# Performance work log

Measured on AMD Instinct MI355X. Metric: run time of the kernel, lower is better.

The kernel has to match this reference:

```python
import jax, jax.numpy as jnp
import numpy as np

HEADS = 8
EPS = 1e-5


def setup_inputs() -> dict:
    key = jax.random.key(0)
    B, N, C = 32, 4096, 256
    headc = C // HEADS
    x = jax.random.normal(key, (B, N, C), dtype=jnp.float32)
    return {
        "x": x,
        "kln_weight": jnp.ones((HEADS, 1, headc), dtype=jnp.float32),
        "kln_bias": jnp.zeros((HEADS, 1, headc), dtype=jnp.float32),
        "vln_weight": jnp.ones((HEADS, 1, headc), dtype=jnp.float32),
        "vln_bias": jnp.zeros((HEADS, 1, headc), dtype=jnp.float32),
    }


def _ln(t, w, b, headc):
    # Faithful to the torch module: unbiased std (ddof=1), eps added to std (not var).
    m = jnp.mean(t, axis=-1, keepdims=True)
    d = t - m
    std = jnp.sqrt(jnp.sum(d * d, axis=-1, keepdims=True) / (headc - 1))
    return w * (d / (std + EPS)) + b


def reference(x, kln_weight, kln_bias, vln_weight, vln_bias):
    B, N, C = x.shape
    headc = C // HEADS
    # [B, H, N, D]
    qkv = x.reshape(B, N, HEADS, headc).transpose(0, 2, 1, 3)
    k = _ln(qkv, kln_weight, kln_bias, headc)
    v = _ln(qkv, vln_weight, vln_bias, headc)
    # k^T v : [B, H, D, D], scaled by 1/N
    kv = jnp.einsum("bhnd,bhne->bhde", k, v) / N
    # q (k^T v): [B, H, N, D]
    out = jnp.einsum("bhnd,bhde->bhne", qkv, kv)
    out = out.transpose(0, 2, 1, 3).reshape(B, N, C)
    return out + x
```

## Files before the change

### kernel.cpp

```cpp
#include <hip/hip_runtime.h>

#define H_ 8
#define D_ 32
#define B_ 32
#define N_ 4096
#define C_ 256
#define EPS_ 1e-5f

#define SLOT_ 1088

typedef __attribute__((ext_vector_type(8))) short bf16x8;
typedef __attribute__((ext_vector_type(4))) float f32x4;

__device__ __forceinline__ short f2bf(float f) {
    unsigned u = __builtin_bit_cast(unsigned, f);
    unsigned r = (u + 0x7FFFu + ((u >> 16) & 1u)) >> 16;
    return (short)r;
}
__device__ __forceinline__ float bf2f(short s) {
    return __builtin_bit_cast(float, ((unsigned)(unsigned short)s) << 16);
}

__device__ __forceinline__ int uidx(int r, int c) {
    return r * 40 + ((r >> 3) & 3) * 16 + c;
}

__global__ __launch_bounds__(256, 4)
void k1_skv(const float* __restrict__ x, float* __restrict__ Pws)
{
    __shared__ short ubuf[256 * 40 + 64];

    const int tid  = threadIdx.x;
    const int bh   = blockIdx.x >> 2;
    const int q4   = blockIdx.x & 3;
    const int b    = bh >> 3;
    const int h    = bh & 7;
    const int lane = tid & 63;
    const int wave = tid >> 6;
    const int g    = lane >> 4;
    const int cL   = lane & 15;

    f32x4 acc[2][2] = {};
    f32x4 tq[2] = {};

    bf16x8 ones;
    #pragma unroll
    for (int j = 0; j < 8; ++j) ones[j] = (short)0x3F80;

    const float* xbase = x + ((size_t)b * N_ + q4 * 1024 + tid) * C_ + h * D_;

    float4 xA[8], xB[8];
    #pragma unroll
    for (int c = 0; c < 8; ++c)
        xA[c] = reinterpret_cast<const float4*>(xbase)[c];

    auto body = [&](const float4 (&xr)[8], float4 (&nx)[8], int it, bool pf) {
        if (pf) {
            const float* p = xbase + (size_t)(it + 1) * 256 * C_;
            #pragma unroll
            for (int c = 0; c < 8; ++c)
                nx[c] = reinterpret_cast<const float4*>(p)[c];
        }

        float sum = 0.f, sq = 0.f;
        #pragma unroll
        for (int c = 0; c < 8; ++c) {
            const float4 a = xr[c];
            sum += a.x + a.y + a.z + a.w;
            sq = fmaf(a.x, a.x, fmaf(a.y, a.y, fmaf(a.z, a.z, fmaf(a.w, a.w, sq))));
        }
        const float m   = sum * (1.f / 32.f);
        const float ss  = fmaxf(sq - sum * m, 0.f);
        const float inv = 1.f / (sqrtf(ss * (1.f / 31.f)) + EPS_);

        {
            const int base = tid * 40 + ((tid >> 3) & 3) * 16;
            #pragma unroll
            for (int q = 0; q < 4; ++q) {
                const float4 a0 = xr[q * 2 + 0];
                const float4 a1 = xr[q * 2 + 1];
                bf16x8 wv;
                wv[0] = f2bf((a0.x - m) * inv); wv[1] = f2bf((a0.y - m) * inv);
                wv[2] = f2bf((a0.z - m) * inv); wv[3] = f2bf((a0.w - m) * inv);
                wv[4] = f2bf((a1.x - m) * inv); wv[5] = f2bf((a1.y - m) * inv);
                wv[6] = f2bf((a1.z - m) * inv); wv[7] = f2bf((a1.w - m) * inv);
                *reinterpret_cast<bf16x8*>(&ubuf[base + q * 8]) = wv;
            }
        }
        asm volatile("s_waitcnt lgkmcnt(0)" ::: "memory");

        #pragma unroll
        for (int ks = 0; ks < 2; ++ks) {
            const int R0 = wave * 64 + ks * 32 + 8 * g;
            bf16x8 F0, F1;
            #pragma unroll
            for (int j = 0; j < 8; ++j) {
                const int base = uidx(R0 + j, cL);
                F0[j] = ubuf[base];
                F1[j] = ubuf[base + 16];
            }
            tq[0] = __builtin_amdgcn_mfma_f32_16x16x32_bf16(ones, F0, tq[0], 0, 0, 0);
            tq[1] = __builtin_amdgcn_mfma_f32_16x16x32_bf16(ones, F1, tq[1], 0, 0, 0);
            acc[0][0] = __builtin_amdgcn_mfma_f32_16x16x32_bf16(F0, F0, acc[0][0], 0, 0, 0);
            acc[0][1] = __builtin_amdgcn_mfma_f32_16x16x32_bf16(F0, F1, acc[0][1], 0, 0, 0);
            acc[1][0] = __builtin_amdgcn_mfma_f32_16x16x32_bf16(F1, F0, acc[1][0], 0, 0, 0);
            acc[1][1] = __builtin_amdgcn_mfma_f32_16x16x32_bf16(F1, F1, acc[1][1], 0, 0, 0);
        }
    };

    body(xA, xB, 0, true);
    body(xB, xA, 1, true);
    body(xA, xB, 2, true);
    body(xB, xA, 3, false);

    __syncthreads();
    float* sred = reinterpret_cast<float*>(ubuf);
    {
        float* dst = sred + wave * 1024;
        #pragma unroll
        for (int ca = 0; ca < 2; ++ca)
            #pragma unroll
            for (int cb = 0; cb < 2; ++cb)
                #pragma unroll
                for (int r = 0; r < 4; ++r)
                    dst[(ca * 16 + g * 4 + r) * D_ + cb * 16 + cL] = acc[ca][cb][r];
    }
    if (lane < 16) {
        sred[4096 + wave * 32 + cL]      = tq[0][0];
        sred[4096 + wave * 32 + 16 + cL] = tq[1][0];
    }
    __syncthreads();

    float* slot = Pws + (size_t)blockIdx.x * SLOT_;
    {
        const float4 c0 = *reinterpret_cast<const float4*>(&sred[tid * 4]);
        const float4 c1 = *reinterpret_cast<const float4*>(&sred[1024 + tid * 4]);
        const float4 c2 = *reinterpret_cast<const float4*>(&sred[2048 + tid * 4]);
        const float4 c3 = *reinterpret_cast<const float4*>(&sred[3072 + tid * 4]);
        float4 o;
        o.x = c0.x + c1.x + c2.x + c3.x;
        o.y = c0.y + c1.y + c2.y + c3.y;
        o.z = c0.z + c1.z + c2.z + c3.z;
        o.w = c0.w + c1.w + c2.w + c3.w;
        *reinterpret_cast<float4*>(slot + tid * 4) = o;
    }
    if (tid < D_)
        slot[1024 + tid] = sred[4096 + tid] + sred[4096 + 32 + tid]
                         + sred[4096 + 64 + tid] + sred[4096 + 96 + tid];
}

__global__ __launch_bounds__(256, 4)
void k_red(const float* __restrict__ Pws,
           const float* __restrict__ kw, const float* __restrict__ kb,
           const float* __restrict__ vw, const float* __restrict__ vb,
           short* __restrict__ kvHi, short* __restrict__ kvLo)
{
    const int bh  = blockIdx.x;
    const int h   = bh & 7;
    const int tid = threadIdx.x;
    const int d   = tid >> 3;
    const int e0  = (tid & 7) * 4;

    const float* P0 = Pws + (size_t)(bh * 4 + 0) * SLOT_;
    const float* P1 = Pws + (size_t)(bh * 4 + 1) * SLOT_;
    const float* P2 = Pws + (size_t)(bh * 4 + 2) * SLOT_;
    const float* P3 = Pws + (size_t)(bh * 4 + 3) * SLOT_;
    const float invN = 1.f / (float)N_;

    const float4 s0 = *reinterpret_cast<const float4*>(P0 + d * D_ + e0);
    const float4 s1 = *reinterpret_cast<const float4*>(P1 + d * D_ + e0);
    const float4 s2 = *reinterpret_cast<const float4*>(P2 + d * D_ + e0);
    const float4 s3 = *reinterpret_cast<const float4*>(P3 + d * D_ + e0);
    float Sde[4] = { s0.x + s1.x + s2.x + s3.x, s0.y + s1.y + s2.y + s3.y,
                     s0.z + s1.z + s2.z + s3.z, s0.w + s1.w + s2.w + s3.w };

    const float Td  = P0[1024 + d] + P1[1024 + d] + P2[1024 + d] + P3[1024 + d];
    const float wkd = kw[h * D_ + d];
    const float bkd = kb[h * D_ + d];

    #pragma unroll
    for (int j = 0; j < 4; ++j) {
        const int e = e0 + j;
        const float Te  = P0[1024 + e] + P1[1024 + e] + P2[1024 + e] + P3[1024 + e];
        const float wve = vw[h * D_ + e];
        const float bve = vb[h * D_ + e];
        float v = invN * (wkd * (wve * Sde[j] + bve * Td) + bkd * wve * Te)
                + bkd * bve;
        if (d == e) v += 1.0f;
        const short hi = f2bf(v);
        const short lo = f2bf(v - bf2f(hi));
        const int hf  = e >> 4;
        const int l   = ((d >> 3) << 4) | (e & 15);
        const int idx = bh * 1024 + hf * 512 + l * 8 + (d & 7);
        kvHi[idx] = hi;
        kvLo[idx] = lo;
    }
}

__global__ __launch_bounds__(256, 4)
void k2_out(const float* __restrict__ x,
            const short* __restrict__ kvHi, const short* __restrict__ kvLo,
            float* __restrict__ out)
{
    const int tid  = threadIdx.x;
    const int lane = tid & 63;
    const int w    = tid >> 6;
    const int g    = lane >> 4;
    const int cL   = lane & 15;
    const int b    = blockIdx.x >> 6;
    const int row  = blockIdx.x * 64 + w * 16 + cL;

    const float* xr   = x + (size_t)row * C_;
    float*       orow = out + (size_t)row * C_;
    const size_t fb   = (size_t)(b * H_) * 1024 + lane * 8;

    const f32x4 zero = {0.f, 0.f, 0.f, 0.f};

    bf16x8 hA0, lA0, hA1, lA1, hB0, lB0, hB1, lB1;
    float4 qA0, qA1, qB0, qB1;

#define LOADH(H, h0, l0, h1, l1, q0, q1)                                      \
    h0 = *reinterpret_cast<const bf16x8*>(kvHi + fb + (H) * 1024);            \
    l0 = *reinterpret_cast<const bf16x8*>(kvLo + fb + (H) * 1024);            \
    h1 = *reinterpret_cast<const bf16x8*>(kvHi + fb + (H) * 1024 + 512);      \
    l1 = *reinterpret_cast<const bf16x8*>(kvLo + fb + (H) * 1024 + 512);      \
    q0 = *reinterpret_cast<const float4*>(xr + (H) * 32 + 8 * g);             \
    q1 = *reinterpret_cast<const float4*>(xr + (H) * 32 + 8 * g + 4);

#define COMPUTE(H, h0, l0, h1, l1, q0, q1)                                    \
    {                                                                         \
        bf16x8 Qb;                                                            \
        Qb[0] = f2bf(q0.x); Qb[1] = f2bf(q0.y);                               \
        Qb[2] = f2bf(q0.z); Qb[3] = f2bf(q0.w);                               \
        Qb[4] = f2bf(q1.x); Qb[5] = f2bf(q1.y);                               \
        Qb[6] = f2bf(q1.z); Qb[7] = f2bf(q1.w);                               \
        f32x4 Dv;                                                             \
        Dv = __builtin_amdgcn_mfma_f32_16x16x32_bf16(l0, Qb, zero, 0, 0, 0);  \
        Dv = __builtin_amdgcn_mfma_f32_16x16x32_bf16(h0, Qb, Dv,   0, 0, 0);  \
        *reinterpret_cast<f32x4*>(orow + (H) * 32 + 4 * g) = Dv;              \
        Dv = __builtin_amdgcn_mfma_f32_16x16x32_bf16(l1, Qb, zero, 0, 0, 0);  \
        Dv = __builtin_amdgcn_mfma_f32_16x16x32_bf16(h1, Qb, Dv,   0, 0, 0);  \
        *reinterpret_cast<f32x4*>(orow + (H) * 32 + 16 + 4 * g) = Dv;         \
    }

    LOADH(0, hA0, lA0, hA1, lA1, qA0, qA1)
    LOADH(1, hB0, lB0, hB1, lB1, qB0, qB1)
    COMPUTE(0, hA0, lA0, hA1, lA1, qA0, qA1)
    LOADH(2, hA0, lA0, hA1, lA1, qA0, qA1)
    COMPUTE(1, hB0, lB0, hB1, lB1, qB0, qB1)
    LOADH(3, hB0, lB0, hB1, lB1, qB0, qB1)
    COMPUTE(2, hA0, lA0, hA1, lA1, qA0, qA1)
    LOADH(4, hA0, lA0, hA1, lA1, qA0, qA1)
    COMPUTE(3, hB0, lB0, hB1, lB1, qB0, qB1)
    LOADH(5, hB0, lB0, hB1, lB1, qB0, qB1)
    COMPUTE(4, hA0, lA0, hA1, lA1, qA0, qA1)
    LOADH(6, hA0, lA0, hA1, lA1, qA0, qA1)
    COMPUTE(5, hB0, lB0, hB1, lB1, qB0, qB1)
    LOADH(7, hB0, lB0, hB1, lB1, qB0, qB1)
    COMPUTE(6, hA0, lA0, hA1, lA1, qA0, qA1)
    COMPUTE(7, hB0, lB0, hB1, lB1, qB0, qB1)

#undef LOADH
#undef COMPUTE
}

extern "C" void kernel_launch(void* const* d_in, const int* in_sizes, int n_in,
                              void* d_out, int out_size, void* d_ws, size_t ws_size,
                              hipStream_t stream)
{
    const float* x  = (const float*)d_in[0];
    const float* kw = (const float*)d_in[1];
    const float* kb = (const float*)d_in[2];
    const float* vw = (const float*)d_in[3];
    const float* vb = (const float*)d_in[4];
    float* outp = (float*)d_out;

    float* Pws  = (float*)d_ws;
    short* kvHi = (short*)(Pws + (size_t)1024 * SLOT_);
    short* kvLo = kvHi + (size_t)256 * 1024;

    k1_skv<<<dim3(B_ * H_ * 4), dim3(256), 0, stream>>>(x, Pws);
    k_red<<<dim3(B_ * H_), dim3(256), 0, stream>>>(Pws, kw, kb, vw, vb, kvHi, kvLo);
    k2_out<<<dim3(B_ * N_ / 64), dim3(256), 0, stream>>>(x, kvHi, kvLo, outp);
}
```

Measured before the change: 84.50 us.

## Stage per-batch KV matrices in LDS and process 128 rows per block

The output kernel now copies the batch's hi/lo bf16 KV matrices into shared memory once per block and reads them from LDS, rather than every wave fetching them from global memory. Each block handles 128 rows instead of 64, and the x loads are restructured into three deep register buffers covering four heads at a time. This cuts redundant global/L2 traffic for KV and deepens memory-level parallelism. In exchange it adds a block-wide sync, 32KB of LDS per block and higher register pressure, with the occupancy hint lowered from 4 to 3.

```diff
diff --git a/kernel.cpp b/kernel.cpp
--- a/kernel.cpp
+++ b/kernel.cpp
@@ -197,70 +197,86 @@
     }
 }
 
-__global__ __launch_bounds__(256, 4)
+__global__ __launch_bounds__(256, 3)
 void k2_out(const float* __restrict__ x,
             const short* __restrict__ kvHi, const short* __restrict__ kvLo,
             float* __restrict__ out)
 {
+    __shared__ short kvL[16384];
+
     const int tid  = threadIdx.x;
     const int lane = tid & 63;
     const int w    = tid >> 6;
     const int g    = lane >> 4;
     const int cL   = lane & 15;
-    const int b    = blockIdx.x >> 6;
-    const int row  = blockIdx.x * 64 + w * 16 + cL;
-
-    const float* xr   = x + (size_t)row * C_;
-    float*       orow = out + (size_t)row * C_;
-    const size_t fb   = (size_t)(b * H_) * 1024 + lane * 8;
+    const int row0 = blockIdx.x * 128;
+    const int b    = blockIdx.x >> 5;
+    const int rowL = row0 + w * 16 + cL;
+
+    {
+        const short* srcH = kvHi + (size_t)b * 8192;
+        const short* srcL = kvLo + (size_t)b * 8192;
+        #pragma unroll
+        for (int i = 0; i < 4; ++i) {
+            const int o = (tid + i * 256) * 8;
+            *reinterpret_cast<bf16x8*>(&kvL[o]) =
+                *reinterpret_cast<const bf16x8*>(srcH + o);
+            *reinterpret_cast<bf16x8*>(&kvL[8192 + o]) =
+                *reinterpret_cast<const bf16x8*>(srcL + o);
+        }
+    }
+    __syncthreads();
 
     const f32x4 zero = {0.f, 0.f, 0.f, 0.f};
 
-    bf16x8 hA0, lA0, hA1, lA1, hB0, lB0, hB1, lB1;
-    float4 qA0, qA1, qB0, qB1;
-
-#define LOADH(H, h0, l0, h1, l1, q0, q1)                                      \
-    h0 = *reinterpret_cast<const bf16x8*>(kvHi + fb + (H) * 1024);            \
-    l0 = *reinterpret_cast<const bf16x8*>(kvLo + fb + (H) * 1024);            \
-    h1 = *reinterpret_cast<const bf16x8*>(kvHi + fb + (H) * 1024 + 512);      \
-    l1 = *reinterpret_cast<const bf16x8*>(kvLo + fb + (H) * 1024 + 512);      \
-    q0 = *reinterpret_cast<const float4*>(xr + (H) * 32 + 8 * g);             \
-    q1 = *reinterpret_cast<const float4*>(xr + (H) * 32 + 8 * g + 4);
-
-#define COMPUTE(H, h0, l0, h1, l1, q0, q1)                                    \
+    float4 qA[8], qB[8], qC[8];
+
+#define LOADQ(HT, Q)                                                          \
     {                                                                         \
-        bf16x8 Qb;                                                            \
-        Qb[0] = f2bf(q0.x); Qb[1] = f2bf(q0.y);                               \
-        Qb[2] = f2bf(q0.z); Qb[3] = f2bf(q0.w);                               \
-        Qb[4] = f2bf(q1.x); Qb[5] = f2bf(q1.y);                               \
-        Qb[6] = f2bf(q1.z); Qb[7] = f2bf(q1.w);                               \
-        f32x4 Dv;                                                             \
-        Dv = __builtin_amdgcn_mfma_f32_16x16x32_bf16(l0, Qb, zero, 0, 0, 0);  \
-        Dv = __builtin_amdgcn_mfma_f32_16x16x32_bf16(h0, Qb, Dv,   0, 0, 0);  \
-        *reinterpret_cast<f32x4*>(orow + (H) * 32 + 4 * g) = Dv;              \
-        Dv = __builtin_amdgcn_mfma_f32_16x16x32_bf16(l1, Qb, zero, 0, 0, 0);  \
-        Dv = __builtin_amdgcn_mfma_f32_16x16x32_bf16(h1, Qb, Dv,   0, 0, 0);  \
-        *reinterpret_cast<f32x4*>(orow + (H) * 32 + 16 + 4 * g) = Dv;         \
-    }
-
-    LOADH(0, hA0, lA0, hA1, lA1, qA0, qA1)
-    LOADH(1, hB0, lB0, hB1, lB1, qB0, qB1)
-    COMPUTE(0, hA0, lA0, hA1, lA1, qA0, qA1)
-    LOADH(2, hA0, lA0, hA1, lA1, qA0, qA1)
-    COMPUTE(1, hB0, lB0, hB1, lB1, qB0, qB1)
-    LOADH(3, hB0, lB0, hB1, lB1, qB0, qB1)
-    COMPUTE(2, hA0, lA0, hA1, lA1, qA0, qA1)
-    LOADH(4, hA0, lA0, hA1, lA1, qA0, qA1)
-    COMPUTE(3, hB0, lB0, hB1, lB1, qB0, qB1)
-    LOADH(5, hB0, lB0, hB1, lB1, qB0, qB1)
-    COMPUTE(4, hA0, lA0, hA1, lA1, qA0, qA1)
-    LOADH(6, hA0, lA0, hA1, lA1, qA0, qA1)
-    COMPUTE(5, hB0, lB0, hB1, lB1, qB0, qB1)
-    LOADH(7, hB0, lB0, hB1, lB1, qB0, qB1)
-    COMPUTE(6, hA0, lA0, hA1, lA1, qA0, qA1)
-    COMPUTE(7, hB0, lB0, hB1, lB1, qB0, qB1)
-
-#undef LOADH
+        const float* xp = x + (size_t)(rowL + ((HT) >> 1) * 64) * C_          \
+                            + ((HT) & 1) * 128 + 8 * g;                       \
+        _Pragma("unroll")                                                     \
+        for (int j = 0; j < 4; ++j) {                                         \
+            Q[2 * j]     = *reinterpret_cast<const float4*>(xp + j * 32);     \
+            Q[2 * j + 1] = *reinterpret_cast<const float4*>(xp + j * 32 + 4); \
+        }                                                                     \
+    }
+
+#define COMPUTE(HT, Q)                                                        \
+    {                                                                         \
+        float* orow = out + (size_t)(rowL + ((HT) >> 1) * 64) * C_;           \
+        _Pragma("unroll")                                                     \
+        for (int j = 0; j < 4; ++j) {                                         \
+            const int h = ((HT) & 1) * 4 + j;                                 \
+            bf16x8 Qb;                                                        \
+            Qb[0] = f2bf(Q[2 * j].x);     Qb[1] = f2bf(Q[2 * j].y);           \
+            Qb[2] = f2bf(Q[2 * j].z);     Qb[3] = f2bf(Q[2 * j].w);           \
+            Qb[4] = f2bf(Q[2 * j + 1].x); Qb[5] = f2bf(Q[2 * j + 1].y);       \
+            Qb[6] = f2bf(Q[2 * j + 1].z); Qb[7] = f2bf(Q[2 * j + 1].w);       \
+            _Pragma("unroll")                                                 \
+            for (int hf = 0; hf < 2; ++hf) {                                  \
+                const int si = h * 1024 + hf * 512 + lane * 8;                \
+                const bf16x8 hi = *reinterpret_cast<const bf16x8*>(&kvL[si]); \
+                const bf16x8 lo =                                             \
+                    *reinterpret_cast<const bf16x8*>(&kvL[8192 + si]);        \
+                f32x4 Dv;                                                     \
+                Dv = __builtin_amdgcn_mfma_f32_16x16x32_bf16(lo, Qb, zero, 0, 0, 0); \
+                Dv = __builtin_amdgcn_mfma_f32_16x16x32_bf16(hi, Qb, Dv,   0, 0, 0); \
+                *reinterpret_cast<f32x4*>(orow + h * 32 + hf * 16 + 4 * g) = Dv;     \
+            }                                                                 \
+        }                                                                     \
+    }
+
+    LOADQ(0, qA)
+    LOADQ(1, qB)
+    LOADQ(2, qC)
+    COMPUTE(0, qA)
+    LOADQ(3, qA)
+    COMPUTE(1, qB)
+    COMPUTE(2, qC)
+    COMPUTE(3, qA)
+
+#undef LOADQ
 #undef COMPUTE
 }
 
@@ -281,5 +297,5 @@
 
     k1_skv<<<dim3(B_ * H_ * 4), dim3(256), 0, stream>>>(x, Pws);
     k_red<<<dim3(B_ * H_), dim3(256), 0, stream>>>(Pws, kw, kb, vw, vb, kvHi, kvLo);
-    k2_out<<<dim3(B_ * N_ / 64), dim3(256), 0, stream>>>(x, kvHi, kvLo, outp);
-}
+    k2_out<<<dim3(B_ * N_ / 128), dim3(256), 0, stream>>>(x, kvHi, kvLo, outp);
+}
```

Result: no change. 84.28 us (-0.3%).
